# Performance work log

Measured on AMD Instinct MI355X. Metric: run time of the kernel, lower is better.

Reference implementation:

```python
import jax, jax.numpy as jnp
import numpy as np

B, C, H, W = 4, 64, 64, 64
CI = C // 2  # inter_channels


def setup_inputs() -> dict:
    key = jax.random.key(0)
    k1, k2, k3, k4, k5 = jax.random.split(key, 5)
    x = jax.random.normal(k1, (B, C, H, W), dtype=jnp.float32)
    # 1x1 conv g: in C -> CI (weight [CI, C], bias [CI])
    Wg = jax.random.normal(k2, (CI, C), dtype=jnp.float32) * (1.0 / np.sqrt(C))
    bg = jax.random.normal(k3, (CI,), dtype=jnp.float32) * 0.01
    # 1x1 conv W_z: CI -> C
    Wz = jax.random.normal(k4, (C, CI), dtype=jnp.float32) * (1.0 / np.sqrt(CI))
    bz = jax.random.normal(k5, (C,), dtype=jnp.float32) * 0.01
    return {"x": x, "Wg": Wg, "bg": bg, "Wz": Wz, "bz": bz}


def reference(x, Wg, bg, Wz, bz):
    b, c, h, w = x.shape
    n = h * w
    xf = x.reshape(b, c, n)                       # [B,C,N]
    # g projection (1x1 conv) then flatten: [B,N,CI]
    g_x = jnp.einsum('bcn,oc->bno', xf, Wg) + bg  # [B,N,CI]
    # theta = phi = raw x flattened
    theta = xf.transpose(0, 2, 1)                 # [B,N,C]
    f = jnp.einsum('bnc,bcm->bnm', theta, xf)     # [B,N,N]
    f_div_C = jax.nn.softmax(f, axis=-1)
    y = jnp.einsum('bnm,bmo->bno', f_div_C, g_x)  # [B,N,CI]
    y = y.transpose(0, 2, 1).reshape(b, CI, h, w)  # [B,CI,H,W]
    # W_z projection (1x1 conv) + residual
    W_y = jnp.einsum('oi,bihw->bohw', Wz, y) + bz[None, :, None, None]
    return W_y + x
```

## Files before the change

kernel.cpp:

```cpp
#include <hip/hip_runtime.h>
#include <hip/hip_bf16.h>
#include <math.h>

#define B_  4
#define C_  64
#define N_  4096
#define CI_ 32

typedef __attribute__((ext_vector_type(8))) unsigned short u16x8;
typedef __attribute__((ext_vector_type(8))) __bf16        bf16x8;
typedef __attribute__((ext_vector_type(4))) float         f32x4;

__device__ __forceinline__ unsigned short f2bf(float f) {
    union { float f; unsigned int i; } v; v.f = f;
    unsigned int r = v.i + 0x7FFFu + ((v.i >> 16) & 1u);
    return (unsigned short)(r >> 16);
}

__global__ __launch_bounds__(256) void k_prep(
    const float* __restrict__ x, const float* __restrict__ Wg,
    const float* __restrict__ bg, unsigned short* __restrict__ xT,
    unsigned short* __restrict__ gx, float* __restrict__ diag)
{
    __shared__ __align__(16) float tile[64][68];
    __shared__ float part[4][64][33];
    const int t  = threadIdx.x;
    const int b  = blockIdx.x >> 6;
    const int n0 = (blockIdx.x & 63) * 64;

    #pragma unroll
    for (int pass = 0; pass < 4; ++pass) {
        int c   = (t >> 4) + pass * 16;
        int nl4 = (t & 15) * 4;
        float4 v = *(const float4*)(x + (size_t)(b * C_ + c) * N_ + n0 + nl4);
        *(float4*)&tile[c][nl4] = v;
    }
    __syncthreads();

    {
        const int n  = t >> 2;
        const int cc = (t & 3) * 16;
        u16x8 a, b2;
        #pragma unroll
        for (int j = 0; j < 8; ++j) a[j]  = f2bf(tile[cc + j][n]);
        #pragma unroll
        for (int j = 0; j < 8; ++j) b2[j] = f2bf(tile[cc + 8 + j][n]);
        unsigned short* dst = xT + (size_t)(b * N_ + n0 + n) * C_ + cc;
        *(u16x8*)dst       = a;
        *(u16x8*)(dst + 8) = b2;
    }
    {
        const int nl = t & 63, cq = t >> 6;
        float acc[CI_];
        #pragma unroll
        for (int o = 0; o < CI_; ++o) acc[o] = 0.f;
        float dd = 0.f;
        #pragma unroll 4
        for (int cl = 0; cl < 16; ++cl) {
            int c = cq * 16 + cl;
            float xv = tile[c][nl];
            dd += xv * xv;
            #pragma unroll
            for (int o = 0; o < CI_; ++o) acc[o] += Wg[o * C_ + c] * xv;
        }
        #pragma unroll
        for (int o = 0; o < CI_; ++o) part[cq][nl][o] = acc[o];
        part[cq][nl][32] = dd;
    }
    __syncthreads();
    {
        const int o = t >> 3, nr = (t & 7) * 8;
        u16x8 w;
        #pragma unroll
        for (int j = 0; j < 8; ++j) {
            int n = nr + j;
            float s = part[0][n][o] + part[1][n][o] + part[2][n][o] + part[3][n][o]
                    + bg[o];
            w[j] = f2bf(s);
        }
        *(u16x8*)(gx + (size_t)(b * CI_ + o) * N_ + n0 + nr) = w;
    }
    if (t < 64)
        diag[(size_t)b * N_ + n0 + t] =
            part[0][t][32] + part[1][t][32] + part[2][t][32] + part[3][t][32];
}

__device__ __forceinline__ f32x4 mfma16(bf16x8 a, bf16x8 b, f32x4 c) {
    return __builtin_amdgcn_mfma_f32_16x16x32_bf16(a, b, c, 0, 0, 0);
}

__global__ __launch_bounds__(256, 3) void k_flash(
    const unsigned short* __restrict__ xT, const unsigned short* __restrict__ gx,
    const float* __restrict__ diag,
    float* __restrict__ ypart, float* __restrict__ lpart)
{
    __shared__ __align__(16) char smem[34816];
    unsigned short* Pl = (unsigned short*)smem;
    float*          ym = (float*)smem;

    const int tid  = threadIdx.x;
    const int wave = tid >> 6, lane = tid & 63;
    const int quad = lane >> 4, li = lane & 15;
    const int bi  = blockIdx.x;
    const int kq  = bi & 3;
    const int qtb = (bi >> 2) & 63;
    const int b   = bi >> 8;
    const int q0  = qtb * 64;

    const unsigned short* xTb = xT + (size_t)b * N_ * C_;
    const unsigned short* gxb = gx + (size_t)(b * CI_) * N_;

    float Kq[4];
    #pragma unroll
    for (int qt = 0; qt < 4; ++qt)
        Kq[qt] = diag[(size_t)b * N_ + q0 + qt * 16 + li];

    bf16x8 Qf[4][2];
    #pragma unroll
    for (int qt = 0; qt < 4; ++qt)
        #pragma unroll
        for (int kc = 0; kc < 2; ++kc)
            Qf[qt][kc] = *(const bf16x8*)(xTb + (size_t)(q0 + qt * 16 + li) * C_
                                          + kc * 32 + quad * 8);

    f32x4 Yf[4][2];
    #pragma unroll
    for (int qt = 0; qt < 4; ++qt)
        #pragma unroll
        for (int ot = 0; ot < 2; ++ot)
            Yf[qt][ot] = (f32x4){0.f, 0.f, 0.f, 0.f};
    float lacc[4] = {0.f, 0.f, 0.f, 0.f};

    const int keybase = kq * 1024 + wave * 256;

    for (int tl = 0; tl < 8; ++tl) {
        const int k0 = keybase + tl * 32;

        bf16x8 A[2][2];
        #pragma unroll
        for (int kt = 0; kt < 2; ++kt)
            #pragma unroll
            for (int kc = 0; kc < 2; ++kc)
                A[kt][kc] = *(const bf16x8*)(xTb + (size_t)(k0 + kt * 16 + li) * C_
                                             + kc * 32 + quad * 8);
        bf16x8 Bv[2];
        #pragma unroll
        for (int ot = 0; ot < 2; ++ot)
            Bv[ot] = *(const bf16x8*)(gxb + (size_t)(ot * 16 + li) * N_
                                      + k0 + quad * 8);

        f32x4 S[2][4];
        #pragma unroll
        for (int kt = 0; kt < 2; ++kt)
            #pragma unroll
            for (int qt = 0; qt < 4; ++qt) {
                f32x4 z = (f32x4){0.f, 0.f, 0.f, 0.f};
                z = mfma16(A[kt][0], Qf[qt][0], z);
                S[kt][qt] = mfma16(A[kt][1], Qf[qt][1], z);
            }

        #pragma unroll
        for (int qt = 0; qt < 4; ++qt) {
            float p[2][4];
            #pragma unroll
            for (int kt = 0; kt < 2; ++kt)
                #pragma unroll
                for (int r = 0; r < 4; ++r) {
                    p[kt][r] = __expf(S[kt][qt][r] - Kq[qt]);
                    lacc[qt] += p[kt][r];
                }
            #pragma unroll
            for (int kt = 0; kt < 2; ++kt) {
                uint2 wv;
                wv.x = (unsigned)f2bf(p[kt][0]) | ((unsigned)f2bf(p[kt][1]) << 16);
                wv.y = (unsigned)f2bf(p[kt][2]) | ((unsigned)f2bf(p[kt][3]) << 16);
                *(uint2*)(Pl + (wave * 64 + qt * 16 + li) * 40 + kt * 16 + quad * 4) = wv;
            }
        }

        #pragma unroll
        for (int qt = 0; qt < 4; ++qt) {
            bf16x8 Ap = *(const bf16x8*)(Pl + (wave * 64 + qt * 16 + li) * 40 + quad * 8);
            #pragma unroll
            for (int ot = 0; ot < 2; ++ot)
                Yf[qt][ot] = mfma16(Ap, Bv[ot], Yf[qt][ot]);
        }
    }

    #pragma unroll
    for (int qt = 0; qt < 4; ++qt) {
        lacc[qt] += __shfl_xor(lacc[qt], 16, 64);
        lacc[qt] += __shfl_xor(lacc[qt], 32, 64);
    }

    __syncthreads();
    #pragma unroll
    for (int qt = 0; qt < 4; ++qt) {
        #pragma unroll
        for (int ot = 0; ot < 2; ++ot)
            #pragma unroll
            for (int r = 0; r < 4; ++r)
                ym[(wave * 64 + qt * 16 + quad * 4 + r) * 34 + ot * 16 + li] = Yf[qt][ot][r];
        if (quad == 0)
            ym[(wave * 64 + qt * 16 + li) * 34 + 32] = lacc[qt];
    }
    __syncthreads();
    {
        const int q = tid >> 2, og = tid & 3;
        const size_t pbase = (size_t)(b * 64 + qtb) * 4 + kq;
        float* yp = ypart + pbase * 2048 + q * 32;
        #pragma unroll
        for (int j = 0; j < 8; ++j) {
            int o = og * 8 + j;
            yp[o] = ym[(0 * 64 + q) * 34 + o] + ym[(1 * 64 + q) * 34 + o]
                  + ym[(2 * 64 + q) * 34 + o] + ym[(3 * 64 + q) * 34 + o];
        }
        if (og == 0)
            lpart[pbase * 64 + q] = ym[(0 * 64 + q) * 34 + 32] + ym[(1 * 64 + q) * 34 + 32]
                                  + ym[(2 * 64 + q) * 34 + 32] + ym[(3 * 64 + q) * 34 + 32];
    }
}

__global__ __launch_bounds__(256) void k_merge(
    const float* __restrict__ ypart, const float* __restrict__ lpart,
    const float* __restrict__ x, const float* __restrict__ Wz,
    const float* __restrict__ bz, float* __restrict__ out)
{
    __shared__ float yfin[64][33];
    const int t   = threadIdx.x;
    const int b   = blockIdx.x >> 6;
    const int qtb = blockIdx.x & 63;
    const int q0  = qtb * 64;

    {
        const int q = t >> 2, og = t & 3;
        const size_t pb = (size_t)(b * 64 + qtb) * 4;
        float l = lpart[(pb + 0) * 64 + q] + lpart[(pb + 1) * 64 + q]
                + lpart[(pb + 2) * 64 + q] + lpart[(pb + 3) * 64 + q];
        float inv = 1.f / l;
        #pragma unroll
        for (int j = 0; j < 8; ++j) {
            int o = og * 8 + j;
            float acc = 0.f;
            #pragma unroll
            for (int kq = 0; kq < 4; ++kq)
                acc += ypart[(pb + kq) * 2048 + q * 32 + o];
            yfin[q][o] = acc * inv;
        }
    }
    __syncthreads();
    {
        const int q = t & 63, c0 = t >> 6;
        #pragma unroll
        for (int i = 0; i < 16; ++i) {
            int cout = c0 + i * 4;
            float acc = bz[cout];
            #pragma unroll
            for (int o = 0; o < CI_; ++o)
                acc += Wz[cout * CI_ + o] * yfin[q][o];
            size_t oidx = (size_t)(b * C_ + cout) * N_ + q0 + q;
            out[oidx] = acc + x[oidx];
        }
    }
}

extern "C" void kernel_launch(void* const* d_in, const int* in_sizes, int n_in,
                              void* d_out, int out_size, void* d_ws, size_t ws_size,
                              hipStream_t stream) {
    (void)in_sizes; (void)n_in; (void)out_size; (void)ws_size;
    const float* x  = (const float*)d_in[0];
    const float* Wg = (const float*)d_in[1];
    const float* bg = (const float*)d_in[2];
    const float* Wz = (const float*)d_in[3];
    const float* bz = (const float*)d_in[4];
    float* out = (float*)d_out;

    unsigned short* xT = (unsigned short*)d_ws;
    unsigned short* gx = (unsigned short*)((char*)d_ws + 2097152);
    float* diag  = (float*)((char*)d_ws + 3145728);
    float* ypart = (float*)((char*)d_ws + 3211264);
    float* lpart = (float*)((char*)d_ws + 11599872);

    hipLaunchKernelGGL(k_prep,  dim3(B_ * (N_ / 64)), dim3(256), 0, stream, x, Wg, bg, xT, gx, diag);
    hipLaunchKernelGGL(k_flash, dim3(B_ * 64 * 4),    dim3(256), 0, stream, xT, gx, diag, ypart, lpart);
    hipLaunchKernelGGL(k_merge, dim3(B_ * 64),        dim3(256), 0, stream, ypart, lpart, x, Wz, bz, out);
}
```

Baseline: 122.1 us.

## Fold log2e into query copy, use exp2 and truncating bf16 pack

The prep kernel now also writes a copy of x pre-scaled by log2(e) for the query operand, plus a log2e-scaled diagonal. The flash kernel seeds the MFMA accumulator with minus that diagonal, so the subtraction disappears and each score needs only a raw exp2. Probabilities are packed to bf16 by truncating with a byte permute instead of rounding, and launch bounds are raised to 4 blocks per CU. The goal is to cut VALU work in the softmax inner loop. The cost is an extra 2 MB workspace write and read, slightly less accurate P from truncation, and tighter register pressure.

```diff
diff --git a/kernel.cpp b/kernel.cpp
--- a/kernel.cpp
+++ b/kernel.cpp
@@ -6,6 +6,7 @@
 #define C_  64
 #define N_  4096
 #define CI_ 32
+#define L2E 1.4426950408889634f
 
 typedef __attribute__((ext_vector_type(8))) unsigned short u16x8;
 typedef __attribute__((ext_vector_type(8))) __bf16        bf16x8;
@@ -20,7 +21,8 @@
 __global__ __launch_bounds__(256) void k_prep(
     const float* __restrict__ x, const float* __restrict__ Wg,
     const float* __restrict__ bg, unsigned short* __restrict__ xT,
-    unsigned short* __restrict__ gx, float* __restrict__ diag)
+    unsigned short* __restrict__ xq, unsigned short* __restrict__ gx,
+    float* __restrict__ diagS)
 {
     __shared__ __align__(16) float tile[64][68];
     __shared__ float part[4][64][33];
@@ -40,14 +42,16 @@
     {
         const int n  = t >> 2;
         const int cc = (t & 3) * 16;
-        u16x8 a, b2;
-        #pragma unroll
-        for (int j = 0; j < 8; ++j) a[j]  = f2bf(tile[cc + j][n]);
-        #pragma unroll
-        for (int j = 0; j < 8; ++j) b2[j] = f2bf(tile[cc + 8 + j][n]);
-        unsigned short* dst = xT + (size_t)(b * N_ + n0 + n) * C_ + cc;
-        *(u16x8*)dst       = a;
-        *(u16x8*)(dst + 8) = b2;
+        u16x8 a, b2, as, bs;
+        #pragma unroll
+        for (int j = 0; j < 8; ++j) {
+            float v0 = tile[cc + j][n], v1 = tile[cc + 8 + j][n];
+            a[j]  = f2bf(v0);        b2[j] = f2bf(v1);
+            as[j] = f2bf(v0 * L2E);  bs[j] = f2bf(v1 * L2E);
+        }
+        size_t off = (size_t)(b * N_ + n0 + n) * C_ + cc;
+        *(u16x8*)(xT + off)     = a;  *(u16x8*)(xT + off + 8) = b2;
+        *(u16x8*)(xq + off)     = as; *(u16x8*)(xq + off + 8) = bs;
     }
     {
         const int nl = t & 63, cq = t >> 6;
@@ -81,17 +85,17 @@
         *(u16x8*)(gx + (size_t)(b * CI_ + o) * N_ + n0 + nr) = w;
     }
     if (t < 64)
-        diag[(size_t)b * N_ + n0 + t] =
-            part[0][t][32] + part[1][t][32] + part[2][t][32] + part[3][t][32];
+        diagS[(size_t)b * N_ + n0 + t] = L2E *
+            (part[0][t][32] + part[1][t][32] + part[2][t][32] + part[3][t][32]);
 }
 
 __device__ __forceinline__ f32x4 mfma16(bf16x8 a, bf16x8 b, f32x4 c) {
     return __builtin_amdgcn_mfma_f32_16x16x32_bf16(a, b, c, 0, 0, 0);
 }
 
-__global__ __launch_bounds__(256, 3) void k_flash(
-    const unsigned short* __restrict__ xT, const unsigned short* __restrict__ gx,
-    const float* __restrict__ diag,
+__global__ __launch_bounds__(256, 4) void k_flash(
+    const unsigned short* __restrict__ xT, const unsigned short* __restrict__ xq,
+    const unsigned short* __restrict__ gx, const float* __restrict__ diagS,
     float* __restrict__ ypart, float* __restrict__ lpart)
 {
     __shared__ __align__(16) char smem[34816];
@@ -108,19 +112,20 @@
     const int q0  = qtb * 64;
 
     const unsigned short* xTb = xT + (size_t)b * N_ * C_;
+    const unsigned short* xqb = xq + (size_t)b * N_ * C_;
     const unsigned short* gxb = gx + (size_t)(b * CI_) * N_;
 
-    float Kq[4];
+    float nKq[4];
     #pragma unroll
     for (int qt = 0; qt < 4; ++qt)
-        Kq[qt] = diag[(size_t)b * N_ + q0 + qt * 16 + li];
+        nKq[qt] = -diagS[(size_t)b * N_ + q0 + qt * 16 + li];
 
     bf16x8 Qf[4][2];
     #pragma unroll
     for (int qt = 0; qt < 4; ++qt)
         #pragma unroll
         for (int kc = 0; kc < 2; ++kc)
-            Qf[qt][kc] = *(const bf16x8*)(xTb + (size_t)(q0 + qt * 16 + li) * C_
+            Qf[qt][kc] = *(const bf16x8*)(xqb + (size_t)(q0 + qt * 16 + li) * C_
                                           + kc * 32 + quad * 8);
 
     f32x4 Yf[4][2];
@@ -154,7 +159,7 @@
         for (int kt = 0; kt < 2; ++kt)
             #pragma unroll
             for (int qt = 0; qt < 4; ++qt) {
-                f32x4 z = (f32x4){0.f, 0.f, 0.f, 0.f};
+                f32x4 z = (f32x4){nKq[qt], nKq[qt], nKq[qt], nKq[qt]};
                 z = mfma16(A[kt][0], Qf[qt][0], z);
                 S[kt][qt] = mfma16(A[kt][1], Qf[qt][1], z);
             }
@@ -166,14 +171,16 @@
             for (int kt = 0; kt < 2; ++kt)
                 #pragma unroll
                 for (int r = 0; r < 4; ++r) {
-                    p[kt][r] = __expf(S[kt][qt][r] - Kq[qt]);
+                    p[kt][r] = __builtin_amdgcn_exp2f(S[kt][qt][r]);
                     lacc[qt] += p[kt][r];
                 }
             #pragma unroll
             for (int kt = 0; kt < 2; ++kt) {
                 uint2 wv;
-                wv.x = (unsigned)f2bf(p[kt][0]) | ((unsigned)f2bf(p[kt][1]) << 16);
-                wv.y = (unsigned)f2bf(p[kt][2]) | ((unsigned)f2bf(p[kt][3]) << 16);
+                wv.x = __builtin_amdgcn_perm(__float_as_uint(p[kt][1]),
+                                             __float_as_uint(p[kt][0]), 0x07060302);
+                wv.y = __builtin_amdgcn_perm(__float_as_uint(p[kt][3]),
+                                             __float_as_uint(p[kt][2]), 0x07060302);
                 *(uint2*)(Pl + (wave * 64 + qt * 16 + li) * 40 + kt * 16 + quad * 4) = wv;
             }
         }
@@ -276,12 +283,16 @@
     float* out = (float*)d_out;
 
     unsigned short* xT = (unsigned short*)d_ws;
-    unsigned short* gx = (unsigned short*)((char*)d_ws + 2097152);
-    float* diag  = (float*)((char*)d_ws + 3145728);
-    float* ypart = (float*)((char*)d_ws + 3211264);
-    float* lpart = (float*)((char*)d_ws + 11599872);
-
-    hipLaunchKernelGGL(k_prep,  dim3(B_ * (N_ / 64)), dim3(256), 0, stream, x, Wg, bg, xT, gx, diag);
-    hipLaunchKernelGGL(k_flash, dim3(B_ * 64 * 4),    dim3(256), 0, stream, xT, gx, diag, ypart, lpart);
-    hipLaunchKernelGGL(k_merge, dim3(B_ * 64),        dim3(256), 0, stream, ypart, lpart, x, Wz, bz, out);
-}
+    unsigned short* xq = (unsigned short*)((char*)d_ws + 2097152);
+    unsigned short* gx = (unsigned short*)((char*)d_ws + 4194304);
+    float* diagS = (float*)((char*)d_ws + 5242880);
+    float* ypart = (float*)((char*)d_ws + 5308416);
+    float* lpart = (float*)((char*)d_ws + 13697024);
+
+    hipLaunchKernelGGL(k_prep,  dim3(B_ * (N_ / 64)), dim3(256), 0, stream,
+                       x, Wg, bg, xT, xq, gx, diagS);
+    hipLaunchKernelGGL(k_flash, dim3(B_ * 64 * 4),    dim3(256), 0, stream,
+                       xT, xq, gx, diagS, ypart, lpart);
+    hipLaunchKernelGGL(k_merge, dim3(B_ * 64),        dim3(256), 0, stream,
+                       ypart, lpart, x, Wz, bz, out);
+}
```

After: 175.9 us. 1.44x slower.
